# Performance work log

Hardware: AMD Instinct MI355X
Metric: run time of the kernel (lower is better)

## Reference

```python
import jax, jax.numpy as jnp
import numpy as np

BATCH, SEQ, D_IN, D_ST = 16, 8192, 64, 128  # in_features=64, out_features(state)=128


def setup_inputs() -> dict:
    key = jax.random.key(0)
    k0, k1, k2, k3 = jax.random.split(key, 4)
    x = jax.random.normal(k0, (BATCH, SEQ, D_IN), dtype=jnp.float32)
    # State-transition matrix A (HiPPO-initialized in the original). We draw a
    # random dense matrix scaled to spectral radius ~0.9 so the 8192-step
    # recurrence stays numerically stable.
    A = jax.random.normal(k1, (D_ST, D_ST), dtype=jnp.float32) * (0.9 / np.sqrt(D_ST))
    Bw = jax.random.normal(k2, (D_ST, D_IN), dtype=jnp.float32) / np.sqrt(D_IN)
    Bb = jnp.zeros((D_ST,), dtype=jnp.float32)  # bias=True on B
    Cw = jax.random.normal(k3, (D_IN, D_ST), dtype=jnp.float32) / np.sqrt(D_ST)
    return {"x": x, "A": A, "Bw": Bw, "Bb": Bb, "Cw": Cw}


def reference(x, A, Bw, Bb, Cw):
    # Discrete linear SSM: h_t = A h_{t-1} + (B x_t + b),  y_t = C h_t
    # Input projection is batched into one big GEMM (not per-step).
    bx = jnp.einsum('bsi,di->bsd', x, Bw) + Bb          # [B,S,D_ST]
    bx_t = jnp.transpose(bx, (1, 0, 2))                  # [S,B,D_ST]

    def step(h, u):
        h = u + h @ A.T                                  # [B,D_ST]
        return h, h

    h0 = jnp.zeros((x.shape[0], A.shape[0]), dtype=x.dtype)
    _, hs = jax.lax.scan(step, h0, bx_t)                 # hs: [S,B,D_ST]
    # Output projection as one big GEMM after the scan.
    y = jnp.einsum('sbd,od->bso', hs, Cw)                # [B,S,D_IN]
    return y
```

## Files before the change

### kernel.cpp

```cpp
#include <hip/hip_runtime.h>


#define SEQ   8192
#define DIN   64
#define LCH   32
#define NCH   (SEQ / LCH)
#define WFULL 48
#define WTOT  112

typedef _Float16 v8h __attribute__((ext_vector_type(8)));
typedef __fp16   v2h __attribute__((ext_vector_type(2)));
typedef float    v4f __attribute__((ext_vector_type(4)));

#define MFMA(a, b, c) __builtin_amdgcn_mfma_f32_16x16x32_f16((a), (b), (c), 0, 0, 0)
#define PKRTZ __builtin_amdgcn_cvt_pkrtz

__device__ __forceinline__ int rho_inv(int p) {
  int m = p >> 4, q = (p >> 2) & 3, r = p & 3;
  int eh = ((r >> 1) << 1) | (m >> 2);
  int e  = (eh << 1) | (r & 1);
  return 32 * (m & 3) + 8 * q + e;
}

__global__ void prep_kernel(const float* __restrict__ A, const float* __restrict__ Bw,
                            const float* __restrict__ Bb, const float* __restrict__ Cw,
                            _Float16* __restrict__ W, float* __restrict__ Bbs) {
  int idx = blockIdx.x * 256 + threadIdx.x;
  float v; int off_hi, off_lo;
  if (idx < 16384) {
    int p = idx >> 7, j = idx & 127;
    v = A[rho_inv(p) * 128 + j]; off_hi = idx; off_lo = idx + 16384;
  } else if (idx < 24576) {
    int i2 = idx - 16384; int p = i2 >> 6, j = i2 & 63;
    v = Bw[rho_inv(p) * 64 + j]; off_hi = 32768 + i2; off_lo = 40960 + i2;
  } else if (idx < 32768) {
    int i2 = idx - 24576;
    v = Cw[i2]; off_hi = 49152 + i2; off_lo = 57344 + i2;
  } else if (idx < 32896) {
    Bbs[idx - 32768] = Bb[rho_inv(idx - 32768)]; return;
  } else return;
  _Float16 hi = (_Float16)v;
  _Float16 lo = (_Float16)(v - (float)hi);
  W[off_hi] = hi; W[off_lo] = lo;
}

__global__ __launch_bounds__(256, 1) void ssm_kernel(
    const float* __restrict__ x, float* __restrict__ y,
    const _Float16* __restrict__ W, const float* __restrict__ Bbs) {
  const int tid = threadIdx.x;
  const int wv  = tid >> 6;
  const int l   = tid & 63;
  const int n   = l & 15;
  const int q   = l >> 4;
  const int c   = blockIdx.x;
  const int t0  = c * LCH, te = t0 + LCH;
  const int ts  = (t0 > WTOT)  ? (t0 - WTOT)  : 0;
  const int tf  = (t0 > WFULL) ? (t0 - WFULL) : 0;

  const _Float16* Ah = W;
  const _Float16* Al = W + 16384;
  const _Float16* Bh = W + 32768;
  const _Float16* Bl = W + 40960;
  const _Float16* Ch = W + 49152;
  const _Float16* Cl = W + 57344;

  v8h afh[2][4], afl[2][4], bwh[2][2], bwl[2][2], cwh[4], cwl[4];
  v4f bb2[2];
#pragma unroll
  for (int i = 0; i < 2; ++i) {
    int row = 16 * (wv + 4 * i) + n;
#pragma unroll
    for (int kt = 0; kt < 4; ++kt) {
      afh[i][kt] = *(const v8h*)(Ah + row * 128 + 32 * kt + 8 * q);
      afl[i][kt] = *(const v8h*)(Al + row * 128 + 32 * kt + 8 * q);
    }
#pragma unroll
    for (int k2 = 0; k2 < 2; ++k2) {
      bwh[i][k2] = *(const v8h*)(Bh + row * 64 + 32 * k2 + 8 * q);
      bwl[i][k2] = *(const v8h*)(Bl + row * 64 + 32 * k2 + 8 * q);
    }
    bb2[i] = *(const v4f*)(Bbs + 16 * (wv + 4 * i) + 4 * q);
  }
  {
    int row = 16 * wv + n;
#pragma unroll
    for (int kt = 0; kt < 4; ++kt) {
      cwh[kt] = *(const v8h*)(Ch + row * 128 + 32 * kt + 8 * q);
      cwl[kt] = *(const v8h*)(Cl + row * 128 + 32 * kt + 8 * q);
    }
  }

  __shared__ _Float16 hx[2][2][4][512];

  const float* xb = x + (size_t)n * (SEQ * DIN) + 8 * q;
  float* yb = y + (size_t)n * (SEQ * DIN);

  v4f bufA[4], bufB[4];
  auto loadx = [&](v4f(&buf)[4], int t) {
    const float* p = xb + (size_t)t * DIN;
    buf[0] = *(const v4f*)(p);
    buf[1] = *(const v4f*)(p + 4);
    buf[2] = *(const v4f*)(p + 32);
    buf[3] = *(const v4f*)(p + 36);
  };

  v8h hf[4], hlo[4];
#pragma unroll
  for (int kt = 0; kt < 4; ++kt) { hf[kt] = v8h{}; hlo[kt] = v8h{}; }

  v4f uA[2], uB[2];

  auto build_u = [&](const v4f(&b)[4], bool full) {
    union { v2h h2[4]; v8h h8; } H0, H1;
    H0.h2[0] = PKRTZ(b[0][0], b[0][1]); H0.h2[1] = PKRTZ(b[0][2], b[0][3]);
    H0.h2[2] = PKRTZ(b[1][0], b[1][1]); H0.h2[3] = PKRTZ(b[1][2], b[1][3]);
    H1.h2[0] = PKRTZ(b[2][0], b[2][1]); H1.h2[1] = PKRTZ(b[2][2], b[2][3]);
    H1.h2[2] = PKRTZ(b[3][0], b[3][1]); H1.h2[3] = PKRTZ(b[3][2], b[3][3]);
    v8h xh0 = H0.h8, xh1 = H1.h8;
#pragma unroll
    for (int i = 0; i < 2; ++i) {
      v4f a = bb2[i];
      a = MFMA(bwh[i][0], xh0, a);
      a = MFMA(bwh[i][1], xh1, a);
      uA[i] = a;
    }
    if (full) {
      float r[16];
#pragma unroll
      for (int i = 0; i < 8; ++i) r[i]     = b[i >> 2][i & 3]       - (float)H0.h8[i];
#pragma unroll
      for (int i = 0; i < 8; ++i) r[8 + i] = b[2 + (i >> 2)][i & 3] - (float)H1.h8[i];
      union { v2h h2[4]; v8h h8; } L0, L1;
      L0.h2[0] = PKRTZ(r[0], r[1]);   L0.h2[1] = PKRTZ(r[2], r[3]);
      L0.h2[2] = PKRTZ(r[4], r[5]);   L0.h2[3] = PKRTZ(r[6], r[7]);
      L1.h2[0] = PKRTZ(r[8], r[9]);   L1.h2[1] = PKRTZ(r[10], r[11]);
      L1.h2[2] = PKRTZ(r[12], r[13]); L1.h2[3] = PKRTZ(r[14], r[15]);
      v8h xl0 = L0.h8, xl1 = L1.h8;
#pragma unroll
      for (int i = 0; i < 2; ++i) {
        v4f a = {0.f, 0.f, 0.f, 0.f};
        a = MFMA(bwl[i][0], xh0, a);
        a = MFMA(bwl[i][1], xh1, a);
        a = MFMA(bwh[i][0], xl0, a);
        a = MFMA(bwh[i][1], xl1, a);
        uB[i] = a;
      }
    }
  };

  auto emit_y = [&](int t) {
    v4f e1 = {0.f,0.f,0.f,0.f}, e2 = {0.f,0.f,0.f,0.f}, e3 = {0.f,0.f,0.f,0.f};
#pragma unroll
    for (int kt = 0; kt < 4; ++kt) e1 = MFMA(cwh[kt], hf[kt],  e1);
#pragma unroll
    for (int kt = 0; kt < 4; ++kt) e2 = MFMA(cwh[kt], hlo[kt], e2);
#pragma unroll
    for (int kt = 0; kt < 4; ++kt) e3 = MFMA(cwl[kt], hf[kt],  e3);
    v4f r = e1 + e2 + e3;
    *(v4f*)(yb + (size_t)t * DIN + 16 * wv + 4 * q) = r;
  };

  auto xwrite = [&](int pr, const v4f& a0, const v4f& a1, bool full) {
    union { v2h h2[4]; v8h h8; } U;
    U.h2[0] = PKRTZ(a0[0], a0[1]); U.h2[1] = PKRTZ(a1[0], a1[1]);
    U.h2[2] = PKRTZ(a0[2], a0[3]); U.h2[3] = PKRTZ(a1[2], a1[3]);
    *(v8h*)&hx[pr][0][wv][l * 8] = U.h8;
    if (full) {
      float r0 = a0[0] - (float)U.h8[0], r1 = a0[1] - (float)U.h8[1];
      float r2 = a1[0] - (float)U.h8[2], r3 = a1[1] - (float)U.h8[3];
      float r4 = a0[2] - (float)U.h8[4], r5 = a0[3] - (float)U.h8[5];
      float r6 = a1[2] - (float)U.h8[6], r7 = a1[3] - (float)U.h8[7];
      union { v2h h2[4]; v8h h8; } L;
      L.h2[0] = PKRTZ(r0, r1); L.h2[1] = PKRTZ(r2, r3);
      L.h2[2] = PKRTZ(r4, r5); L.h2[3] = PKRTZ(r6, r7);
      *(v8h*)&hx[pr][1][wv][l * 8] = L.h8;
    }
  };

  auto step_full = [&](int t, v4f(&bsrc)[4], v4f(&bld)[4], int pr, bool emit) {
    if (emit) emit_y(t - 1);
    v4f c1[2], c2[2], c3[2];
#pragma unroll
    for (int i = 0; i < 2; ++i) {
      c1[i] = uA[i]; c2[i] = uB[i]; c3[i] = v4f{0.f, 0.f, 0.f, 0.f};
    }
#pragma unroll
    for (int kt = 0; kt < 4; ++kt)
#pragma unroll
      for (int i = 0; i < 2; ++i) {
        c1[i] = MFMA(afh[i][kt], hf[kt],  c1[i]);
        c2[i] = MFMA(afl[i][kt], hf[kt],  c2[i]);
        c3[i] = MFMA(afh[i][kt], hlo[kt], c3[i]);
      }
    build_u(bsrc, true);
    int tn = t + 2; if (tn > SEQ - 1) tn = SEQ - 1;
    loadx(bld, tn);
    v4f a0 = c1[0] + c2[0] + c3[0];
    v4f a1 = c1[1] + c2[1] + c3[1];
    xwrite(pr, a0, a1, true);
    __syncthreads();
#pragma unroll
    for (int kt = 0; kt < 4; ++kt) {
      hf[kt]  = *(const v8h*)&hx[pr][0][kt][l * 8];
      hlo[kt] = *(const v8h*)&hx[pr][1][kt][l * 8];
    }
  };

  auto step_cheap = [&](int t, v4f(&bsrc)[4], v4f(&bld)[4], int pr) {
    v4f c1[2];
#pragma unroll
    for (int i = 0; i < 2; ++i) c1[i] = uA[i];
#pragma unroll
    for (int kt = 0; kt < 4; ++kt)
#pragma unroll
      for (int i = 0; i < 2; ++i) c1[i] = MFMA(afh[i][kt], hf[kt], c1[i]);
    build_u(bsrc, (t + 1) >= tf);
    loadx(bld, t + 2);
    xwrite(pr, c1[0], c1[1], false);
    __syncthreads();
#pragma unroll
    for (int kt = 0; kt < 4; ++kt) hf[kt] = *(const v8h*)&hx[pr][0][kt][l * 8];
  };

  loadx(bufA, ts);
  loadx(bufB, ts + 1);
  build_u(bufA, ts >= tf);

  for (int t = ts; t < tf; t += 2) {
    step_cheap(t,     bufB, bufA, 0);
    step_cheap(t + 1, bufA, bufB, 1);
  }
  for (int t = tf; t < t0; t += 2) {
    step_full(t,     bufB, bufA, 0, false);
    step_full(t + 1, bufA, bufB, 1, false);
  }
  for (int t = t0; t < te; t += 2) {
    step_full(t,     bufB, bufA, 0, t > t0);
    step_full(t + 1, bufA, bufB, 1, true);
  }
  emit_y(te - 1);
}

extern "C" void kernel_launch(void* const* d_in, const int* in_sizes, int n_in,
                              void* d_out, int out_size, void* d_ws, size_t ws_size,
                              hipStream_t stream) {
  const float* x  = (const float*)d_in[0];
  const float* A  = (const float*)d_in[1];
  const float* Bw = (const float*)d_in[2];
  const float* Bb = (const float*)d_in[3];
  const float* Cw = (const float*)d_in[4];
  float* y = (float*)d_out;

  _Float16* W   = (_Float16*)d_ws;
  float*    Bbs = (float*)(W + 65536);

  prep_kernel<<<129, 256, 0, stream>>>(A, Bw, Bb, Cw, W, Bbs);
  ssm_kernel<<<NCH, 256, 0, stream>>>(x, y, W, Bbs);
}
```

Before: 102.3 us.

## Warm up chunk state with 4-step strided recurrence using precomputed A^4

Each block's warm-up prefix is now run with a 4-step jump: prep kernels precompute A^2, A^4, and the matching A^k·Bw input terms and fused bias. The warm-up then takes one matvec with A^4 per four timesteps, cutting the length of the serial dependency chain and the number of block barriers. MFMA accumulator chains are also split into independent partial sums to shorten dependency latency. The cost is an extra prep kernel doing naive fp32 matrix powers, more registers for the warm-up weights, and possible accuracy drift from compounding the powered matrix in split-fp16 arithmetic.

```diff
diff --git a/kernel.cpp b/kernel.cpp
--- a/kernel.cpp
+++ b/kernel.cpp
@@ -14,7 +14,15 @@
 
 #define MFMA(a, b, c) __builtin_amdgcn_mfma_f32_16x16x32_f16((a), (b), (c), 0, 0, 0)
 #define PKRTZ __builtin_amdgcn_cvt_pkrtz
-
+#define Z4 (v4f{0.f, 0.f, 0.f, 0.f})
+
+__device__ __forceinline__ int rho_fwd(int lidx) {
+  int kt = lidx >> 5, q = (lidx >> 3) & 3, e = lidx & 7;
+  int eh = e >> 1;
+  int m = kt + 4 * (eh & 1);
+  int r = 2 * (eh >> 1) + (e & 1);
+  return 16 * m + 4 * q + r;
+}
 __device__ __forceinline__ int rho_inv(int p) {
   int m = p >> 4, q = (p >> 2) & 3, r = p & 3;
   int eh = ((r >> 1) << 1) | (m >> 2);
@@ -22,31 +30,113 @@
   return 32 * (m & 3) + 8 * q + e;
 }
 
-__global__ void prep_kernel(const float* __restrict__ A, const float* __restrict__ Bw,
-                            const float* __restrict__ Bb, const float* __restrict__ Cw,
-                            _Float16* __restrict__ W, float* __restrict__ Bbs) {
+__device__ __forceinline__ void pack_hl(float v, _Float16* hp, _Float16* lp) {
+  _Float16 h = (_Float16)v;
+  *hp = h; *lp = (_Float16)(v - (float)h);
+}
+
+
+__global__ void prep1(const float* __restrict__ A, const float* __restrict__ Bw,
+                      const float* __restrict__ Bb, const float* __restrict__ Cw,
+                      _Float16* __restrict__ F, float* __restrict__ Bbs,
+                      float* __restrict__ A2f, float* __restrict__ U1f,
+                      float* __restrict__ b1f) {
   int idx = blockIdx.x * 256 + threadIdx.x;
-  float v; int off_hi, off_lo;
   if (idx < 16384) {
-    int p = idx >> 7, j = idx & 127;
-    v = A[rho_inv(p) * 128 + j]; off_hi = idx; off_lo = idx + 16384;
+    int i = idx >> 7, j = idx & 127;
+    float s = 0.f; const float* ar = A + i * 128;
+    for (int k = 0; k < 128; ++k) s = fmaf(ar[k], A[k * 128 + j], s);
+    A2f[idx] = s;
   } else if (idx < 24576) {
-    int i2 = idx - 16384; int p = i2 >> 6, j = i2 & 63;
-    v = Bw[rho_inv(p) * 64 + j]; off_hi = 32768 + i2; off_lo = 40960 + i2;
+    int p = idx - 16384; int i = p >> 6, j = p & 63;
+    float s = 0.f; const float* ar = A + i * 128;
+    for (int k = 0; k < 128; ++k) s = fmaf(ar[k], Bw[k * 64 + j], s);
+    U1f[p] = s;
+  } else if (idx < 24704) {
+    int i = idx - 24576;
+    float s = 0.f; const float* ar = A + i * 128;
+    for (int k = 0; k < 128; ++k) s = fmaf(ar[k], Bb[k], s);
+    b1f[i] = s;
+  } else if (idx < 41088) {
+    int p = idx - 24704; int i = p >> 7, j = p & 127;
+    int o = rho_fwd(i) * 128 + j;
+    pack_hl(A[p], F + o, F + 16384 + o);
+  } else if (idx < 49280) {
+    int p = idx - 41088; int i = p >> 6, j = p & 63;
+    int o = rho_fwd(i) * 64 + j;
+    pack_hl(Bw[p], F + 65536 + 3 * 8192 + o, F + 98304 + 3 * 8192 + o);
+  } else if (idx < 57472) {
+    int p = idx - 49280;
+    pack_hl(Cw[p], F + 131072 + p, F + 139264 + p);
+  } else if (idx < 57600) {
+    int i = idx - 57472;
+    Bbs[i] = Bb[rho_inv(i)];
+  }
+}
+
+__global__ void prep2(const float* __restrict__ Bw, const float* __restrict__ Bb,
+                      _Float16* __restrict__ F, float* __restrict__ Bb4s,
+                      const float* __restrict__ A2f, const float* __restrict__ U1f,
+                      const float* __restrict__ b1f) {
+  int idx = blockIdx.x * 256 + threadIdx.x;
+  if (idx < 16384) {
+    int i = idx >> 7, j = idx & 127;
+    float s = 0.f; const float* ar = A2f + i * 128;
+    for (int k = 0; k < 128; ++k) s = fmaf(ar[k], A2f[k * 128 + j], s);
+    int o = rho_fwd(i) * 128 + j;
+    pack_hl(s, F + 32768 + o, F + 49152 + o);
+  } else if (idx < 24576) {
+    int p = idx - 16384; int i = p >> 6, j = p & 63;
+    float s = 0.f; const float* ar = A2f + i * 128;
+    for (int k = 0; k < 128; ++k) s = fmaf(ar[k], Bw[k * 64 + j], s);
+    int o = rho_fwd(i) * 64 + j;
+    pack_hl(s, F + 65536 + 8192 + o, F + 98304 + 8192 + o);
   } else if (idx < 32768) {
-    int i2 = idx - 24576;
-    v = Cw[i2]; off_hi = 49152 + i2; off_lo = 57344 + i2;
+    int p = idx - 24576; int i = p >> 6, j = p & 63;
+    float s = 0.f; const float* ar = A2f + i * 128;
+    for (int k = 0; k < 128; ++k) s = fmaf(ar[k], U1f[k * 64 + j], s);
+    int o = rho_fwd(i) * 64 + j;
+    pack_hl(s, F + 65536 + o, F + 98304 + o);
   } else if (idx < 32896) {
-    Bbs[idx - 32768] = Bb[rho_inv(idx - 32768)]; return;
-  } else return;
-  _Float16 hi = (_Float16)v;
-  _Float16 lo = (_Float16)(v - (float)hi);
-  W[off_hi] = hi; W[off_lo] = lo;
+    int i = idx - 32768;
+    float s = Bb[i] + b1f[i];
+    const float* ar = A2f + i * 128;
+    for (int k = 0; k < 128; ++k) s = fmaf(ar[k], Bb[k] + b1f[k], s);
+    Bb4s[rho_fwd(i)] = s;
+  } else if (idx < 41088) {
+    int p = idx - 32896; int i = p >> 6, j = p & 63;
+    int o = rho_fwd(i) * 64 + j;
+    pack_hl(U1f[p], F + 65536 + 2 * 8192 + o, F + 98304 + 2 * 8192 + o);
+  }
+}
+
+__device__ __forceinline__ void split16(const v4f* b, v8h& xh0, v8h& xh1,
+                                        v8h& xl0, v8h& xl1, bool full) {
+  union { v2h h2[4]; v8h h8; } H0, H1;
+  H0.h2[0] = PKRTZ(b[0][0], b[0][1]); H0.h2[1] = PKRTZ(b[0][2], b[0][3]);
+  H0.h2[2] = PKRTZ(b[1][0], b[1][1]); H0.h2[3] = PKRTZ(b[1][2], b[1][3]);
+  H1.h2[0] = PKRTZ(b[2][0], b[2][1]); H1.h2[1] = PKRTZ(b[2][2], b[2][3]);
+  H1.h2[2] = PKRTZ(b[3][0], b[3][1]); H1.h2[3] = PKRTZ(b[3][2], b[3][3]);
+  xh0 = H0.h8; xh1 = H1.h8;
+  if (full) {
+    float r[16];
+#pragma unroll
+    for (int i = 0; i < 8; ++i) r[i]     = b[i >> 2][i & 3]       - (float)H0.h8[i];
+#pragma unroll
+    for (int i = 0; i < 8; ++i) r[8 + i] = b[2 + (i >> 2)][i & 3] - (float)H1.h8[i];
+    union { v2h h2[4]; v8h h8; } L0, L1;
+    L0.h2[0] = PKRTZ(r[0], r[1]);   L0.h2[1] = PKRTZ(r[2], r[3]);
+    L0.h2[2] = PKRTZ(r[4], r[5]);   L0.h2[3] = PKRTZ(r[6], r[7]);
+    L1.h2[0] = PKRTZ(r[8], r[9]);   L1.h2[1] = PKRTZ(r[10], r[11]);
+    L1.h2[2] = PKRTZ(r[12], r[13]); L1.h2[3] = PKRTZ(r[14], r[15]);
+    xl0 = L0.h8; xl1 = L1.h8;
+  }
 }
 
 __global__ __launch_bounds__(256, 1) void ssm_kernel(
     const float* __restrict__ x, float* __restrict__ y,
-    const _Float16* __restrict__ W, const float* __restrict__ Bbs) {
+    const _Float16* __restrict__ F, const float* __restrict__ Bbs,
+    const float* __restrict__ Bb4s) {
   const int tid = threadIdx.x;
   const int wv  = tid >> 6;
   const int l   = tid & 63;
@@ -56,109 +146,25 @@
   const int t0  = c * LCH, te = t0 + LCH;
   const int ts  = (t0 > WTOT)  ? (t0 - WTOT)  : 0;
   const int tf  = (t0 > WFULL) ? (t0 - WFULL) : 0;
-
-  const _Float16* Ah = W;
-  const _Float16* Al = W + 16384;
-  const _Float16* Bh = W + 32768;
-  const _Float16* Bl = W + 40960;
-  const _Float16* Ch = W + 49152;
-  const _Float16* Cl = W + 57344;
-
-  v8h afh[2][4], afl[2][4], bwh[2][2], bwl[2][2], cwh[4], cwl[4];
-  v4f bb2[2];
-#pragma unroll
-  for (int i = 0; i < 2; ++i) {
-    int row = 16 * (wv + 4 * i) + n;
-#pragma unroll
-    for (int kt = 0; kt < 4; ++kt) {
-      afh[i][kt] = *(const v8h*)(Ah + row * 128 + 32 * kt + 8 * q);
-      afl[i][kt] = *(const v8h*)(Al + row * 128 + 32 * kt + 8 * q);
-    }
-#pragma unroll
-    for (int k2 = 0; k2 < 2; ++k2) {
-      bwh[i][k2] = *(const v8h*)(Bh + row * 64 + 32 * k2 + 8 * q);
-      bwl[i][k2] = *(const v8h*)(Bl + row * 64 + 32 * k2 + 8 * q);
-    }
-    bb2[i] = *(const v4f*)(Bbs + 16 * (wv + 4 * i) + 4 * q);
-  }
-  {
-    int row = 16 * wv + n;
-#pragma unroll
-    for (int kt = 0; kt < 4; ++kt) {
-      cwh[kt] = *(const v8h*)(Ch + row * 128 + 32 * kt + 8 * q);
-      cwl[kt] = *(const v8h*)(Cl + row * 128 + 32 * kt + 8 * q);
-    }
-  }
+  const int nwarm = (t0 - ts) >> 2;
+
+  const _Float16* Ah = F;
+  const _Float16* Al = F + 16384;
+  const _Float16* Ph = F + 32768;
+  const _Float16* Pl = F + 49152;
+  const _Float16* Uh = F + 65536;
+  const _Float16* Ul = F + 98304;
+  const _Float16* Ch = F + 131072;
+  const _Float16* Cl = F + 139264;
 
   __shared__ _Float16 hx[2][2][4][512];
 
   const float* xb = x + (size_t)n * (SEQ * DIN) + 8 * q;
   float* yb = y + (size_t)n * (SEQ * DIN);
 
-  v4f bufA[4], bufB[4];
-  auto loadx = [&](v4f(&buf)[4], int t) {
-    const float* p = xb + (size_t)t * DIN;
-    buf[0] = *(const v4f*)(p);
-    buf[1] = *(const v4f*)(p + 4);
-    buf[2] = *(const v4f*)(p + 32);
-    buf[3] = *(const v4f*)(p + 36);
-  };
-
   v8h hf[4], hlo[4];
 #pragma unroll
   for (int kt = 0; kt < 4; ++kt) { hf[kt] = v8h{}; hlo[kt] = v8h{}; }
-
-  v4f uA[2], uB[2];
-
-  auto build_u = [&](const v4f(&b)[4], bool full) {
-    union { v2h h2[4]; v8h h8; } H0, H1;
-    H0.h2[0] = PKRTZ(b[0][0], b[0][1]); H0.h2[1] = PKRTZ(b[0][2], b[0][3]);
-    H0.h2[2] = PKRTZ(b[1][0], b[1][1]); H0.h2[3] = PKRTZ(b[1][2], b[1][3]);
-    H1.h2[0] = PKRTZ(b[2][0], b[2][1]); H1.h2[1] = PKRTZ(b[2][2], b[2][3]);
-    H1.h2[2] = PKRTZ(b[3][0], b[3][1]); H1.h2[3] = PKRTZ(b[3][2], b[3][3]);
-    v8h xh0 = H0.h8, xh1 = H1.h8;
-#pragma unroll
-    for (int i = 0; i < 2; ++i) {
-      v4f a = bb2[i];
-      a = MFMA(bwh[i][0], xh0, a);
-      a = MFMA(bwh[i][1], xh1, a);
-      uA[i] = a;
-    }
-    if (full) {
-      float r[16];
-#pragma unroll
-      for (int i = 0; i < 8; ++i) r[i]     = b[i >> 2][i & 3]       - (float)H0.h8[i];
-#pragma unroll
-      for (int i = 0; i < 8; ++i) r[8 + i] = b[2 + (i >> 2)][i & 3] - (float)H1.h8[i];
-      union { v2h h2[4]; v8h h8; } L0, L1;
-      L0.h2[0] = PKRTZ(r[0], r[1]);   L0.h2[1] = PKRTZ(r[2], r[3]);
-      L0.h2[2] = PKRTZ(r[4], r[5]);   L0.h2[3] = PKRTZ(r[6], r[7]);
-      L1.h2[0] = PKRTZ(r[8], r[9]);   L1.h2[1] = PKRTZ(r[10], r[11]);
-      L1.h2[2] = PKRTZ(r[12], r[13]); L1.h2[3] = PKRTZ(r[14], r[15]);
-      v8h xl0 = L0.h8, xl1 = L1.h8;
-#pragma unroll
-      for (int i = 0; i < 2; ++i) {
-        v4f a = {0.f, 0.f, 0.f, 0.f};
-        a = MFMA(bwl[i][0], xh0, a);
-        a = MFMA(bwl[i][1], xh1, a);
-        a = MFMA(bwh[i][0], xl0, a);
-        a = MFMA(bwh[i][1], xl1, a);
-        uB[i] = a;
-      }
-    }
-  };
-
-  auto emit_y = [&](int t) {
-    v4f e1 = {0.f,0.f,0.f,0.f}, e2 = {0.f,0.f,0.f,0.f}, e3 = {0.f,0.f,0.f,0.f};
-#pragma unroll
-    for (int kt = 0; kt < 4; ++kt) e1 = MFMA(cwh[kt], hf[kt],  e1);
-#pragma unroll
-    for (int kt = 0; kt < 4; ++kt) e2 = MFMA(cwh[kt], hlo[kt], e2);
-#pragma unroll
-    for (int kt = 0; kt < 4; ++kt) e3 = MFMA(cwl[kt], hf[kt],  e3);
-    v4f r = e1 + e2 + e3;
-    *(v4f*)(yb + (size_t)t * DIN + 16 * wv + 4 * q) = r;
-  };
 
   auto xwrite = [&](int pr, const v4f& a0, const v4f& a1, bool full) {
     union { v2h h2[4]; v8h h8; } U;
@@ -177,27 +183,195 @@
     }
   };
 
+  if (nwarm > 0) {
+    v8h pfh[2][4], pfl[2][4], uwh[4][2][2], uwl[4][2][2];
+    v4f bb4[2];
+#pragma unroll
+    for (int i = 0; i < 2; ++i) {
+      int row = 16 * (wv + 4 * i) + n;
+#pragma unroll
+      for (int kt = 0; kt < 4; ++kt) {
+        pfh[i][kt] = *(const v8h*)(Ph + row * 128 + 32 * kt + 8 * q);
+        pfl[i][kt] = *(const v8h*)(Pl + row * 128 + 32 * kt + 8 * q);
+      }
+#pragma unroll
+      for (int d = 0; d < 4; ++d)
+#pragma unroll
+        for (int k2 = 0; k2 < 2; ++k2) {
+          uwh[d][i][k2] = *(const v8h*)(Uh + d * 8192 + row * 64 + 32 * k2 + 8 * q);
+          uwl[d][i][k2] = *(const v8h*)(Ul + d * 8192 + row * 64 + 32 * k2 + 8 * q);
+        }
+      bb4[i] = *(const v4f*)(Bb4s + 16 * (wv + 4 * i) + 4 * q);
+    }
+
+    v4f xw[4][4];
+    v4f u4A[2], u4B[2];
+    auto loadx4 = [&](int tt) {
+#pragma unroll
+      for (int d = 0; d < 4; ++d) {
+        const float* p = xb + (size_t)(tt + d) * DIN;
+        xw[d][0] = *(const v4f*)(p);
+        xw[d][1] = *(const v4f*)(p + 4);
+        xw[d][2] = *(const v4f*)(p + 32);
+        xw[d][3] = *(const v4f*)(p + 36);
+      }
+    };
+    auto build_u4 = [&](bool full) {
+      v4f a1[2] = {bb4[0], bb4[1]};
+      v4f a2[2] = {Z4, Z4};
+      v4f b1v[2] = {Z4, Z4};
+      v4f b2v[2] = {Z4, Z4};
+#pragma unroll
+      for (int d = 0; d < 4; ++d) {
+        v8h xh0, xh1, xl0, xl1;
+        split16(xw[d], xh0, xh1, xl0, xl1, full);
+        v4f* ta = (d < 2) ? a1 : a2;
+        v4f* tb = (d < 2) ? b1v : b2v;
+#pragma unroll
+        for (int i = 0; i < 2; ++i) {
+          ta[i] = MFMA(uwh[d][i][0], xh0, ta[i]);
+          ta[i] = MFMA(uwh[d][i][1], xh1, ta[i]);
+          if (full) {
+            tb[i] = MFMA(uwl[d][i][0], xh0, tb[i]);
+            tb[i] = MFMA(uwl[d][i][1], xh1, tb[i]);
+            tb[i] = MFMA(uwh[d][i][0], xl0, tb[i]);
+            tb[i] = MFMA(uwh[d][i][1], xl1, tb[i]);
+          }
+        }
+      }
+#pragma unroll
+      for (int i = 0; i < 2; ++i) { u4A[i] = a1[i] + a2[i]; u4B[i] = b1v[i] + b2v[i]; }
+    };
+
+    loadx4(ts);
+    build_u4(ts >= tf);
+    loadx4(ts + 4);
+
+    for (int j = 0; j < nwarm; ++j) {
+      const int  pr    = j & 1;
+      const bool fullj = (ts + 4 * j) >= tf;
+      v4f acc[2];
+#pragma unroll
+      for (int i = 0; i < 2; ++i) {
+        v4f a = MFMA(pfh[i][0], hf[0], u4A[i]);
+        a     = MFMA(pfh[i][1], hf[1], a);
+        v4f b = MFMA(pfh[i][2], hf[2], Z4);
+        b     = MFMA(pfh[i][3], hf[3], b);
+        if (fullj) {
+          v4f c2a = MFMA(pfl[i][0], hf[0], u4B[i]);
+          c2a     = MFMA(pfl[i][1], hf[1], c2a);
+          v4f c2b = MFMA(pfl[i][2], hf[2], Z4);
+          c2b     = MFMA(pfl[i][3], hf[3], c2b);
+          v4f c3a = MFMA(pfh[i][0], hlo[0], Z4);
+          c3a     = MFMA(pfh[i][1], hlo[1], c3a);
+          v4f c3b = MFMA(pfh[i][2], hlo[2], Z4);
+          c3b     = MFMA(pfh[i][3], hlo[3], c3b);
+          acc[i] = (a + b) + (c2a + c2b) + (c3a + c3b);
+        } else {
+          acc[i] = a + b;
+        }
+      }
+      if (j + 1 < nwarm) {
+        build_u4((ts + 4 * (j + 1)) >= tf);
+        loadx4(ts + 4 * (j + 2));
+      }
+      xwrite(pr, acc[0], acc[1], fullj);
+      __syncthreads();
+#pragma unroll
+      for (int kt = 0; kt < 4; ++kt) hf[kt] = *(const v8h*)&hx[pr][0][kt][l * 8];
+      if (fullj) {
+#pragma unroll
+        for (int kt = 0; kt < 4; ++kt) hlo[kt] = *(const v8h*)&hx[pr][1][kt][l * 8];
+      }
+    }
+  }
+
+  asm volatile("" ::: "memory");
+
+  v8h afh[2][4], afl[2][4], bwh[2][2], bwl[2][2], cwh[4], cwl[4];
+  v4f bb2[2];
+#pragma unroll
+  for (int i = 0; i < 2; ++i) {
+    int row = 16 * (wv + 4 * i) + n;
+#pragma unroll
+    for (int kt = 0; kt < 4; ++kt) {
+      afh[i][kt] = *(const v8h*)(Ah + row * 128 + 32 * kt + 8 * q);
+      afl[i][kt] = *(const v8h*)(Al + row * 128 + 32 * kt + 8 * q);
+    }
+#pragma unroll
+    for (int k2 = 0; k2 < 2; ++k2) {
+      bwh[i][k2] = *(const v8h*)(Uh + 3 * 8192 + row * 64 + 32 * k2 + 8 * q);
+      bwl[i][k2] = *(const v8h*)(Ul + 3 * 8192 + row * 64 + 32 * k2 + 8 * q);
+    }
+    bb2[i] = *(const v4f*)(Bbs + 16 * (wv + 4 * i) + 4 * q);
+  }
+  {
+    int row = 16 * wv + n;
+#pragma unroll
+    for (int kt = 0; kt < 4; ++kt) {
+      cwh[kt] = *(const v8h*)(Ch + row * 128 + 32 * kt + 8 * q);
+      cwl[kt] = *(const v8h*)(Cl + row * 128 + 32 * kt + 8 * q);
+    }
+  }
+
+  v4f bufA[4], bufB[4];
+  v4f uA[2], uB[2];
+  auto loadx = [&](v4f(&buf)[4], int t) {
+    const float* p = xb + (size_t)t * DIN;
+    buf[0] = *(const v4f*)(p);
+    buf[1] = *(const v4f*)(p + 4);
+    buf[2] = *(const v4f*)(p + 32);
+    buf[3] = *(const v4f*)(p + 36);
+  };
+  auto build_u = [&](const v4f(&b)[4]) {
+    v8h xh0, xh1, xl0, xl1;
+    split16(b, xh0, xh1, xl0, xl1, true);
+#pragma unroll
+    for (int i = 0; i < 2; ++i) {
+      v4f a = bb2[i];
+      a = MFMA(bwh[i][0], xh0, a);
+      a = MFMA(bwh[i][1], xh1, a);
+      uA[i] = a;
+      v4f bacc = MFMA(bwl[i][0], xh0, Z4);
+      bacc = MFMA(bwl[i][1], xh1, bacc);
+      v4f bacc2 = MFMA(bwh[i][0], xl0, Z4);
+      bacc2 = MFMA(bwh[i][1], xl1, bacc2);
+      uB[i] = bacc + bacc2;
+    }
+  };
+  auto emit_y = [&](int t) {
+    v4f e1a = MFMA(cwh[1], hf[1], MFMA(cwh[0], hf[0], Z4));
+    v4f e1b = MFMA(cwh[3], hf[3], MFMA(cwh[2], hf[2], Z4));
+    v4f e2a = MFMA(cwh[1], hlo[1], MFMA(cwh[0], hlo[0], Z4));
+    v4f e2b = MFMA(cwh[3], hlo[3], MFMA(cwh[2], hlo[2], Z4));
+    v4f e3a = MFMA(cwl[1], hf[1], MFMA(cwl[0], hf[0], Z4));
+    v4f e3b = MFMA(cwl[3], hf[3], MFMA(cwl[2], hf[2], Z4));
+    v4f r = (e1a + e1b) + (e2a + e2b) + (e3a + e3b);
+    *(v4f*)(yb + (size_t)t * DIN + 16 * wv + 4 * q) = r;
+  };
   auto step_full = [&](int t, v4f(&bsrc)[4], v4f(&bld)[4], int pr, bool emit) {
     if (emit) emit_y(t - 1);
-    v4f c1[2], c2[2], c3[2];
+    v4f acc[2];
 #pragma unroll
     for (int i = 0; i < 2; ++i) {
-      c1[i] = uA[i]; c2[i] = uB[i]; c3[i] = v4f{0.f, 0.f, 0.f, 0.f};
-    }
-#pragma unroll
-    for (int kt = 0; kt < 4; ++kt)
-#pragma unroll
-      for (int i = 0; i < 2; ++i) {
-        c1[i] = MFMA(afh[i][kt], hf[kt],  c1[i]);
-        c2[i] = MFMA(afl[i][kt], hf[kt],  c2[i]);
-        c3[i] = MFMA(afh[i][kt], hlo[kt], c3[i]);
-      }
-    build_u(bsrc, true);
+      v4f a = MFMA(afh[i][0], hf[0], uA[i]);
+      a     = MFMA(afh[i][1], hf[1], a);
+      v4f b = MFMA(afh[i][2], hf[2], Z4);
+      b     = MFMA(afh[i][3], hf[3], b);
+      v4f c2a = MFMA(afl[i][0], hf[0], uB[i]);
+      c2a     = MFMA(afl[i][1], hf[1], c2a);
+      v4f c2b = MFMA(afl[i][2], hf[2], Z4);
+      c2b     = MFMA(afl[i][3], hf[3], c2b);
+      v4f c3a = MFMA(afh[i][0], hlo[0], Z4);
+      c3a     = MFMA(afh[i][1], hlo[1], c3a);
+      v4f c3b = MFMA(afh[i][2], hlo[2], Z4);
+      c3b     = MFMA(afh[i][3], hlo[3], c3b);
+      acc[i] = (a + b) + (c2a + c2b) + (c3a + c3b);
+    }
+    build_u(bsrc);
     int tn = t + 2; if (tn > SEQ - 1) tn = SEQ - 1;
     loadx(bld, tn);
-    v4f a0 = c1[0] + c2[0] + c3[0];
-    v4f a1 = c1[1] + c2[1] + c3[1];
-    xwrite(pr, a0, a1, true);
+    xwrite(pr, acc[0], acc[1], true);
     __syncthreads();
 #pragma unroll
     for (int kt = 0; kt < 4; ++kt) {
@@ -206,34 +380,9 @@
     }
   };
 
-  auto step_cheap = [&](int t, v4f(&bsrc)[4], v4f(&bld)[4], int pr) {
-    v4f c1[2];
-#pragma unroll
-    for (int i = 0; i < 2; ++i) c1[i] = uA[i];
-#pragma unroll
-    for (int kt = 0; kt < 4; ++kt)
-#pragma unroll
-      for (int i = 0; i < 2; ++i) c1[i] = MFMA(afh[i][kt], hf[kt], c1[i]);
-    build_u(bsrc, (t + 1) >= tf);
-    loadx(bld, t + 2);
-    xwrite(pr, c1[0], c1[1], false);
-    __syncthreads();
-#pragma unroll
-    for (int kt = 0; kt < 4; ++kt) hf[kt] = *(const v8h*)&hx[pr][0][kt][l * 8];
-  };
-
-  loadx(bufA, ts);
-  loadx(bufB, ts + 1);
-  build_u(bufA, ts >= tf);
-
-  for (int t = ts; t < tf; t += 2) {
-    step_cheap(t,     bufB, bufA, 0);
-    step_cheap(t + 1, bufA, bufB, 1);
-  }
-  for (int t = tf; t < t0; t += 2) {
-    step_full(t,     bufB, bufA, 0, false);
-    step_full(t + 1, bufA, bufB, 1, false);
-  }
+  loadx(bufA, t0);
+  loadx(bufB, t0 + 1);
+  build_u(bufA);
   for (int t = t0; t < te; t += 2) {
     step_full(t,     bufB, bufA, 0, t > t0);
     step_full(t + 1, bufA, bufB, 1, true);
@@ -251,9 +400,14 @@
   const float* Cw = (const float*)d_in[4];
   float* y = (float*)d_out;
 
-  _Float16* W   = (_Float16*)d_ws;
-  float*    Bbs = (float*)(W + 65536);
-
-  prep_kernel<<<129, 256, 0, stream>>>(A, Bw, Bb, Cw, W, Bbs);
-  ssm_kernel<<<NCH, 256, 0, stream>>>(x, y, W, Bbs);
-}
+  _Float16* F    = (_Float16*)d_ws;
+  float*    Bbs  = (float*)(F + 147456);
+  float*    Bb4s = Bbs + 128;
+  float*    A2f  = Bb4s + 128;
+  float*    U1f  = A2f + 16384;
+  float*    b1f  = U1f + 8192;
+
+  prep1<<<225, 256, 0, stream>>>(A, Bw, Bb, Cw, F, Bbs, A2f, U1f, b1f);
+  prep2<<<161, 256, 0, stream>>>(Bw, Bb, F, Bb4s, A2f, U1f, b1f);
+  ssm_kernel<<<NCH, 256, 0, stream>>>(x, y, F, Bbs, Bb4s);
+}
```

Result: slower. 126.5 us (+23.6%).
